# Performance work log

Measured on AMD Instinct MI355X. Metric: run time of the kernel, lower is better.

## Reference

```python
import jax, jax.numpy as jnp
import numpy as np

M, D, A, H, N = 400000, 256, 64, 8, 50000
NEG_SLOPE = 0.2


def setup_inputs() -> dict:
    key = jax.random.key(0)
    ks = jax.random.split(key, 8)
    msg = jax.random.normal(ks[0], (M, D), dtype=jnp.float32)
    index = jax.random.randint(ks[1], (M,), 0, N, dtype=jnp.int32)
    t = jax.random.uniform(ks[2], (M,), dtype=jnp.float32)
    scale = 1.0 / np.sqrt(D).astype(np.float32)
    # per-head Linear(D, A, bias=False) weights, stacked: [H, D, A]
    Wq = jax.random.normal(ks[3], (H, D, A), dtype=jnp.float32) * scale
    Wk = jax.random.normal(ks[4], (H, D, A), dtype=jnp.float32) * scale
    Wv = jax.random.normal(ks[5], (H, D, A), dtype=jnp.float32) * scale
    # out_layer: Linear(H*A, D) with bias
    Wout = jax.random.normal(ks[6], (H * A, D), dtype=jnp.float32) * (1.0 / np.sqrt(H * A).astype(np.float32))
    bout = jax.random.normal(ks[7], (D,), dtype=jnp.float32) * 0.01
    return {"msg": msg, "index": index, "t": t, "dim_size": N,
            "Wq": Wq, "Wk": Wk, "Wv": Wv, "Wout": Wout, "bout": bout}


def _segment_attention(msg, index, dim_size, Wq, Wk, Wv, Wout, bout):
    # per-head projections, all heads at once: [m, H, A]
    q = jnp.einsum('md,hda->mha', msg, Wq)
    k = jnp.einsum('md,hda->mha', msg, Wk)
    v = jnp.einsum('md,hda->mha', msg, Wv)
    # per-head dot-product score: [m, H]
    scores = jnp.sum(q * k, axis=-1)
    scores = jnp.where(scores >= 0, scores, NEG_SLOPE * scores)  # leaky_relu
    # scatter softmax over node segments
    seg_max = jax.ops.segment_max(scores, index, num_segments=dim_size)  # [N, H]
    seg_max = jnp.where(jnp.isfinite(seg_max), seg_max, 0.0)  # empty segments
    e = jnp.exp(scores - seg_max[index])  # [m, H]
    seg_sum = jax.ops.segment_sum(e, index, num_segments=dim_size)  # [N, H]
    attn = e / seg_sum[index]  # [m, H]
    # weighted scatter-sum of values -> [N, H, A]
    out_h = jax.ops.segment_sum(v * attn[..., None], index, num_segments=dim_size)
    # concat heads (head-major order matches torch.cat over head list)
    out = out_h.reshape(dim_size, H * A)
    return out @ Wout + bout  # [N, D]


def reference(msg, index, t, dim_size, Wq, Wk, Wv, Wout, bout):
    # t is accepted but unused, matching the original forward
    return _segment_attention(msg, index, dim_size, Wq, Wk, Wv, Wout, bout)
```

## Files before the change

### kernel.cpp

```cpp
#include <hip/hip_runtime.h>
#include <hip/hip_bf16.h>

typedef _Float16 half8 __attribute__((ext_vector_type(8)));
typedef _Float16 half4 __attribute__((ext_vector_type(4)));
typedef float f32x4 __attribute__((ext_vector_type(4)));


#define MFMA16(a, b, c) __builtin_amdgcn_mfma_f32_16x16x32_f16(a, b, c, 0, 0, 0)

__global__ void k_prep(const float* __restrict__ Wq, const float* __restrict__ Wk,
                       const float* __restrict__ Wv, const float* __restrict__ Wout,
                       _Float16* __restrict__ wqkT, _Float16* __restrict__ CT,
                       const int* __restrict__ index, int* __restrict__ counts, int M)
{
    const int b = blockIdx.x;
    const int t = threadIdx.x;
    if (b < 512) {
        int gid = b * 256 + t;
        int h = gid >> 14;
        int d = (gid >> 6) & 255;
        int a = gid & 63;
        int k0 = d >> 5, lk = (d >> 3) & 3, j = d & 7;
        int cb = a >> 4, lr = a & 15;
        int idx = ((k0 * 4 + cb) * 64 + lk * 16 + lr) * 8 + j;
        wqkT[h * 16384 + idx]       = (_Float16)Wq[gid];
        wqkT[(8 + h) * 16384 + idx] = (_Float16)Wk[gid];
    } else if (b < 1024) {
        __shared__ float wv[4][64];
        int bb = b - 512;
        int h = bb >> 6, din0 = (bb & 63) << 2;
        wv[t >> 6][t & 63] = Wv[((h << 8) + din0 + (t >> 6)) * 64 + (t & 63)];
        __syncthreads();
        float s[4] = {0.f, 0.f, 0.f, 0.f};
        for (int a = 0; a < 64; ++a) {
            float wo = Wout[(h * 64 + a) * 256 + t];
            #pragma unroll
            for (int dd = 0; dd < 4; ++dd) s[dd] += wv[dd][a] * wo;
        }
        int nb = t >> 4, lr = t & 15;
        #pragma unroll
        for (int dd = 0; dd < 4; ++dd) {
            int din = din0 + dd;
            int k0 = din >> 5, lk = (din >> 3) & 3, j = din & 7;
            CT[(size_t)((nb * 8 + h) * 8 + k0) * 512 + (lk * 16 + lr) * 8 + j] = (_Float16)s[dd];
        }
    } else {
        int m = (b - 1024) * 256 + t;
        if (m < M) atomicAdd(&counts[index[m]], 1);
    }
}

__global__ __launch_bounds__(1024) void k_scan1(const int* __restrict__ counts,
                                                int* __restrict__ starts,
                                                int* __restrict__ blocktot, int N) {
    __shared__ int s[1024];
    int b = blockIdx.x, t = threadIdx.x;
    int i = b * 1024 + t;
    int x = (i < N) ? counts[i] : 0;
    s[t] = x;
    __syncthreads();
    #pragma unroll
    for (int off = 1; off < 1024; off <<= 1) {
        int v = (t >= off) ? s[t - off] : 0;
        __syncthreads();
        s[t] += v;
        __syncthreads();
    }
    if (i < N) starts[i] = s[t] - x;
    if (t == 1023) blocktot[b] = s[1023];
}

__global__ void k_scan2(const int* __restrict__ blocktot, int* __restrict__ blockoff, int NC) {
    if (threadIdx.x == 0 && blockIdx.x == 0) {
        int run = 0;
        for (int i = 0; i < NC; ++i) { blockoff[i] = run; run += blocktot[i]; }
    }
}

__global__ __launch_bounds__(1024) void k_scan3(int* __restrict__ starts,
                                                int* __restrict__ cursor,
                                                const int* __restrict__ blockoff,
                                                int N, int M) {
    int b = blockIdx.x, t = threadIdx.x;
    int i = b * 1024 + t;
    if (i < N) {
        int v = starts[i] + blockoff[b];
        starts[i] = v;
        cursor[i] = v;
    }
    if (b == 0 && t == 0) starts[N] = M;
}

__global__ void k_scatteridx(const int* __restrict__ index, int* __restrict__ cursor,
                             int* __restrict__ sorted, int* __restrict__ segsorted, int M) {
    int m = blockIdx.x * 256 + threadIdx.x;
    if (m < M) {
        int idx = index[m];
        int pos = atomicAdd(&cursor[idx], 1);
        sorted[pos] = m;
        segsorted[pos] = idx;
    }
}

__global__ __launch_bounds__(256) void k_zero_bnd(const int* __restrict__ segsorted,
                                                  float* __restrict__ u, int M) {
    long r0 = (long)blockIdx.x * 128;
    int g0 = segsorted[r0];
    int g1 = segsorted[r0 + 127];
    int t = threadIdx.x;
    float4 z = {0.f, 0.f, 0.f, 0.f};
    float4* p0 = (float4*)(u + (long)g0 * 2048);
    float4* p1 = (float4*)(u + (long)g1 * 2048);
    p0[t] = z; p0[t + 256] = z;
    p1[t] = z; p1[t + 256] = z;
}

__device__ __forceinline__ void flush_u(float* __restrict__ u, float* __restrict__ segsum,
                                        int g, int gl0, int ghi, int h, int l,
                                        f32x4 a0, float se)
{
    bool bd = (g == gl0) || (g == ghi);
    float* d0 = u + (long)g * 2048 + h * 256 + l * 4;
    if (bd) {
        atomicAdd(d0 + 0, a0[0]); atomicAdd(d0 + 1, a0[1]);
        atomicAdd(d0 + 2, a0[2]); atomicAdd(d0 + 3, a0[3]);
    } else {
        __builtin_nontemporal_store(a0, (f32x4*)d0);
    }
    if (l == 0) {
        float* ds = segsum + (long)g * 8 + h;
        if (bd) atomicAdd(ds, se); else *ds = se;
    }
}

__global__ __launch_bounds__(512) void k_score_wsum(
    const float* __restrict__ msg, const int* __restrict__ sorted,
    const int* __restrict__ segsorted, const _Float16* __restrict__ wqkT,
    float* __restrict__ u, float* __restrict__ segsum, int M)
{
    __shared__ __align__(16) _Float16 At[128 * 256];
    __shared__ float e_lds[128][9];
    __shared__ int s_id[128];
    __shared__ int s_sg[128];
    char* ldsA = (char*)At;
    const int t = threadIdx.x;

    int nwg = gridDim.x;
    int qc = nwg >> 3, rc = nwg & 7;
    int xcd = blockIdx.x & 7, ofs = blockIdx.x >> 3;
    int blk = ((xcd < rc) ? xcd * (qc + 1) : rc * (qc + 1) + (xcd - rc) * qc) + ofs;
    const long m0 = (long)blk * 128;

    if (t < 128) {
        s_id[t] = sorted[m0 + t];
        s_sg[t] = segsorted[m0 + t];
    }
    __syncthreads();

    const f32x4* msgf4 = (const f32x4*)msg;
    #pragma unroll
    for (int it = 0; it < 16; ++it) {
        int e4 = it * 512 + t;
        int row = e4 >> 6, c4 = e4 & 63;
        f32x4 v = __builtin_nontemporal_load(msgf4 + (long)s_id[row] * 64 + c4);
        half4 hv = {(_Float16)v[0], (_Float16)v[1], (_Float16)v[2], (_Float16)v[3]};
        int bb = ((row << 9) + (c4 << 3)) ^ ((row & 7) << 4);
        *(half4*)(ldsA + bb) = hv;
    }
    __syncthreads();

    const int w = t >> 6, l = t & 63, lr = l & 15, lk = l >> 4;
    const int rh = w & 1;
    const int hp = w >> 1;
    const f32x4 zero = {0.f, 0.f, 0.f, 0.f};

    #pragma unroll 1
    for (int hh = 0; hh < 2; ++hh) {
        const int h = hp + hh * 4;
        const _Float16* wq = wqkT + (size_t)h * 16384;
        const _Float16* wk = wqkT + (size_t)(8 + h) * 16384;

        #pragma unroll 1
        for (int pa = 0; pa < 2; ++pa) {
            const int r0 = rh * 64 + pa * 32 + lr;
            const int r1 = r0 + 16;
            f32x4 pq0 = zero, pq1 = zero;
            __builtin_amdgcn_s_setprio(1);
            #pragma unroll 1
            for (int cb = 0; cb < 4; ++cb) {
                f32x4 aq0 = zero, aq1 = zero, ak0 = zero, ak1 = zero;
                #pragma unroll
                for (int k0 = 0; k0 < 8; ++k0) {
                    int c = k0 * 64 + lk * 16;
                    half8 a0 = *(const half8*)(ldsA + (((r0 << 9) + c) ^ ((r0 & 7) << 4)));
                    half8 a1 = *(const half8*)(ldsA + (((r1 << 9) + c) ^ ((r1 & 7) << 4)));
                    half8 bq = *(const half8*)(wq + ((k0 * 4 + cb) * 64 + l) * 8);
                    half8 bk = *(const half8*)(wk + ((k0 * 4 + cb) * 64 + l) * 8);
                    aq0 = MFMA16(a0, bq, aq0);
                    ak0 = MFMA16(a0, bk, ak0);
                    aq1 = MFMA16(a1, bq, aq1);
                    ak1 = MFMA16(a1, bk, ak1);
                }
                pq0 += aq0 * ak0;
                pq1 += aq1 * ak1;
            }
            __builtin_amdgcn_s_setprio(0);
            #pragma unroll
            for (int off = 1; off < 16; off <<= 1) {
                pq0[0] += __shfl_xor(pq0[0], off); pq0[1] += __shfl_xor(pq0[1], off);
                pq0[2] += __shfl_xor(pq0[2], off); pq0[3] += __shfl_xor(pq0[3], off);
                pq1[0] += __shfl_xor(pq1[0], off); pq1[1] += __shfl_xor(pq1[1], off);
                pq1[2] += __shfl_xor(pq1[2], off); pq1[3] += __shfl_xor(pq1[3], off);
            }
            if (lr == 0) {
                int rb = rh * 64 + pa * 32 + lk * 4;
                #pragma unroll
                for (int j = 0; j < 4; ++j) {
                    float s0 = pq0[j];
                    s0 = (s0 >= 0.f) ? s0 : 0.2f * s0;
                    e_lds[rb + j][h] = __expf(s0);
                    float s1 = pq1[j];
                    s1 = (s1 >= 0.f) ? s1 : 0.2f * s1;
                    e_lds[rb + 16 + j][h] = __expf(s1);
                }
            }
        }
    }
    __syncthreads();

    const int gl0 = s_sg[0], ghi = s_sg[127];
    f32x4 a0 = zero;
    float se = 0.f;
    int cur = gl0;

    #pragma unroll 4
    for (int row = 0; row < 128; ++row) {
        int sg = s_sg[row];
        if (sg != cur) {
            flush_u(u, segsum, cur, gl0, ghi, w, l, a0, se);
            cur = sg; a0 = zero; se = 0.f;
        }
        int bb = ((row << 9) + (l << 3)) ^ ((row & 7) << 4);
        half4 mv = *(const half4*)(ldsA + bb);
        float e = e_lds[row][w];
        a0[0] += e * (float)mv[0];
        a0[1] += e * (float)mv[1];
        a0[2] += e * (float)mv[2];
        a0[3] += e * (float)mv[3];
        se += e;
    }
    flush_u(u, segsum, cur, gl0, ghi, w, l, a0, se);
}

__global__ __launch_bounds__(256, 2) void k_out3(
    const float* __restrict__ u, const float* __restrict__ segsum,
    const _Float16* __restrict__ CT, const float* __restrict__ bout,
    float* __restrict__ out, int N)
{
    const int t = threadIdx.x;
    const int w = t >> 6, l = t & 63, lr = l & 15, lk = l >> 4;
    const long r0 = ((long)blockIdx.x * 4 + w) * 32;
    if (r0 >= N) return;

    const f32x4 zero = {0.f, 0.f, 0.f, 0.f};
    f32x4 ac0[16], ac1[16];
    #pragma unroll
    for (int nb = 0; nb < 16; ++nb) { ac0[nb] = zero; ac1[nb] = zero; }

    long rlo = r0 + lr;      if (rlo > N - 1) rlo = N - 1;
    long rhi = r0 + 16 + lr; if (rhi > N - 1) rhi = N - 1;
    const float* ulo = u + rlo * 2048;
    const float* uhi = u + rhi * 2048;
    const float* sslo = segsum + rlo * 8;
    const float* sshi = segsum + rhi * 8;

    #pragma unroll 1
    for (int kc = 0; kc < 8; ++kc) {
        float s0 = sslo[kc];
        float i0 = (s0 > 0.f) ? 1.f / s0 : 0.f;
        float s1 = sshi[kc];
        float i1 = (s1 > 0.f) ? 1.f / s1 : 0.f;
        #pragma unroll
        for (int k0 = 0; k0 < 8; ++k0) {
            const f32x4* p0 = (const f32x4*)(ulo + kc * 256 + k0 * 32 + lk * 8);
            const f32x4* p1 = (const f32x4*)(uhi + kc * 256 + k0 * 32 + lk * 8);
            f32x4 ua = __builtin_nontemporal_load(p0);
            f32x4 ub = __builtin_nontemporal_load(p0 + 1);
            f32x4 uc = __builtin_nontemporal_load(p1);
            f32x4 ud = __builtin_nontemporal_load(p1 + 1);
            half8 alo = {(_Float16)(ua[0] * i0), (_Float16)(ua[1] * i0),
                         (_Float16)(ua[2] * i0), (_Float16)(ua[3] * i0),
                         (_Float16)(ub[0] * i0), (_Float16)(ub[1] * i0),
                         (_Float16)(ub[2] * i0), (_Float16)(ub[3] * i0)};
            half8 ahi = {(_Float16)(uc[0] * i1), (_Float16)(uc[1] * i1),
                         (_Float16)(uc[2] * i1), (_Float16)(uc[3] * i1),
                         (_Float16)(ud[0] * i1), (_Float16)(ud[1] * i1),
                         (_Float16)(ud[2] * i1), (_Float16)(ud[3] * i1)};
            __builtin_amdgcn_s_setprio(1);
            #pragma unroll
            for (int nb = 0; nb < 16; ++nb) {
                half8 b = *(const half8*)(CT + (size_t)((nb * 8 + kc) * 8 + k0) * 512 + l * 8);
                ac0[nb] = MFMA16(alo, b, ac0[nb]);
                ac1[nb] = MFMA16(ahi, b, ac1[nb]);
            }
            __builtin_amdgcn_s_setprio(0);
        }
    }

    #pragma unroll
    for (int nb = 0; nb < 16; ++nb) {
        int col = nb * 16 + lr;
        float bb = bout[col];
        #pragma unroll
        for (int j = 0; j < 4; ++j) {
            long row = r0 + lk * 4 + j;
            if (row < N) out[row * 256 + col] = ac0[nb][j] + bb;
            long row2 = r0 + 16 + lk * 4 + j;
            if (row2 < N) out[row2 * 256 + col] = ac1[nb][j] + bb;
        }
    }
}

extern "C" void kernel_launch(void* const* d_in, const int* in_sizes, int n_in,
                              void* d_out, int out_size, void* d_ws, size_t ws_size,
                              hipStream_t stream)
{
    const float* msg   = (const float*)d_in[0];
    const int*   index = (const int*)d_in[1];
    const float* Wq    = (const float*)d_in[4];
    const float* Wk    = (const float*)d_in[5];
    const float* Wv    = (const float*)d_in[6];
    const float* Wout  = (const float*)d_in[7];
    const float* bout  = (const float*)d_in[8];
    float* out = (float*)d_out;

    const int M = in_sizes[0] / 256;
    const int N = out_size / 256;
    const int NC = (N + 1023) / 1024;

    char* ws = (char*)d_ws;
    _Float16* wqkT = (_Float16*)(ws);
    _Float16* CT   = (_Float16*)(ws + 524288);
    size_t o2 = 1572864;
    float* segsum = (float*)(ws + o2);
    int* counts   = (int*)(ws + o2 + (size_t)N * 32);
    size_t uoff   = (o2 + (size_t)N * 36 + 255) & ~(size_t)255;
    float* u      = (float*)(ws + uoff);
    size_t p2     = uoff + (size_t)N * 8192;
    int* cursor    = (int*)(ws + p2);
    int* starts    = (int*)(ws + p2 + (size_t)N * 4);
    char* p3       = ws + p2 + (((size_t)N * 8 + 4 + 63) & ~(size_t)63);
    int* sorted    = (int*)(p3);
    int* segsorted = (int*)(p3 + (size_t)M * 4);
    int* blocktot  = (int*)(p3 + (size_t)M * 8);
    int* blockoff  = (int*)(p3 + (size_t)M * 8 + 256);

    hipMemsetAsync(ws + o2, 0, (size_t)N * 36, stream);

    k_prep<<<1024 + (M + 255) / 256, 256, 0, stream>>>(Wq, Wk, Wv, Wout, wqkT, CT,
                                                       index, counts, M);
    k_scan1<<<NC, 1024, 0, stream>>>(counts, starts, blocktot, N);
    k_scan2<<<1, 64, 0, stream>>>(blocktot, blockoff, NC);
    k_scan3<<<NC, 1024, 0, stream>>>(starts, cursor, blockoff, N, M);
    k_scatteridx<<<(M + 255) / 256, 256, 0, stream>>>(index, cursor, sorted, segsorted, M);
    k_zero_bnd<<<M / 128, 256, 0, stream>>>(segsorted, u, M);
    k_score_wsum<<<M / 128, 512, 0, stream>>>(msg, sorted, segsorted, wqkT, u, segsum, M);
    k_out3<<<(N + 127) / 128, 256, 0, stream>>>(u, segsum, CT, bout, out, N);
}
```

Measured before the change: 778.7 us.

## Fold boundary zeroing into scatter and assign one head per wave

Removes the separate boundary-zeroing kernel by having the scatter thread at a tile boundary position zero the segment's accumulator row. It also remaps score computation so each wave handles one head over all rows, which removes the head loop and the block barrier before the weighted sum. The cost is that the zeroing is now done serially by single threads, and the score and weighted-sum phases rely on the same wave producing and consuming its head's exp values.

Result: slower. 878.9 us (+12.9%).

```diff
diff --git a/kernel.cpp b/kernel.cpp
--- a/kernel.cpp
+++ b/kernel.cpp
@@ -92,27 +92,22 @@
 }
 
 __global__ void k_scatteridx(const int* __restrict__ index, int* __restrict__ cursor,
-                             int* __restrict__ sorted, int* __restrict__ segsorted, int M) {
+                             int* __restrict__ sorted, int* __restrict__ segsorted,
+                             float* __restrict__ u, int M) {
     int m = blockIdx.x * 256 + threadIdx.x;
     if (m < M) {
         int idx = index[m];
         int pos = atomicAdd(&cursor[idx], 1);
         sorted[pos] = m;
         segsorted[pos] = idx;
-    }
-}
-
-__global__ __launch_bounds__(256) void k_zero_bnd(const int* __restrict__ segsorted,
-                                                  float* __restrict__ u, int M) {
-    long r0 = (long)blockIdx.x * 128;
-    int g0 = segsorted[r0];
-    int g1 = segsorted[r0 + 127];
-    int t = threadIdx.x;
-    float4 z = {0.f, 0.f, 0.f, 0.f};
-    float4* p0 = (float4*)(u + (long)g0 * 2048);
-    float4* p1 = (float4*)(u + (long)g1 * 2048);
-    p0[t] = z; p0[t + 256] = z;
-    p1[t] = z; p1[t + 256] = z;
+        int pl = pos & 127;
+        if (pl == 0 || pl == 127) {
+            f32x4 z = {0.f, 0.f, 0.f, 0.f};
+            f32x4* p = (f32x4*)(u + (long)idx * 2048);
+            #pragma unroll
+            for (int i = 0; i < 512; ++i) p[i] = z;
+        }
+    }
 }
 
 __device__ __forceinline__ void flush_u(float* __restrict__ u, float* __restrict__ segsum,
@@ -170,63 +165,55 @@
     __syncthreads();
 
     const int w = t >> 6, l = t & 63, lr = l & 15, lk = l >> 4;
-    const int rh = w & 1;
-    const int hp = w >> 1;
     const f32x4 zero = {0.f, 0.f, 0.f, 0.f};
+    const _Float16* wq = wqkT + (size_t)w * 16384;
+    const _Float16* wk = wqkT + (size_t)(8 + w) * 16384;
 
     #pragma unroll 1
-    for (int hh = 0; hh < 2; ++hh) {
-        const int h = hp + hh * 4;
-        const _Float16* wq = wqkT + (size_t)h * 16384;
-        const _Float16* wk = wqkT + (size_t)(8 + h) * 16384;
-
+    for (int pa = 0; pa < 4; ++pa) {
+        const int r0 = pa * 32 + lr;
+        const int r1 = r0 + 16;
+        f32x4 pq0 = zero, pq1 = zero;
+        __builtin_amdgcn_s_setprio(1);
         #pragma unroll 1
-        for (int pa = 0; pa < 2; ++pa) {
-            const int r0 = rh * 64 + pa * 32 + lr;
-            const int r1 = r0 + 16;
-            f32x4 pq0 = zero, pq1 = zero;
-            __builtin_amdgcn_s_setprio(1);
-            #pragma unroll 1
-            for (int cb = 0; cb < 4; ++cb) {
-                f32x4 aq0 = zero, aq1 = zero, ak0 = zero, ak1 = zero;
-                #pragma unroll
-                for (int k0 = 0; k0 < 8; ++k0) {
-                    int c = k0 * 64 + lk * 16;
-                    half8 a0 = *(const half8*)(ldsA + (((r0 << 9) + c) ^ ((r0 & 7) << 4)));
-                    half8 a1 = *(const half8*)(ldsA + (((r1 << 9) + c) ^ ((r1 & 7) << 4)));
-                    half8 bq = *(const half8*)(wq + ((k0 * 4 + cb) * 64 + l) * 8);
-                    half8 bk = *(const half8*)(wk + ((k0 * 4 + cb) * 64 + l) * 8);
-                    aq0 = MFMA16(a0, bq, aq0);
-                    ak0 = MFMA16(a0, bk, ak0);
-                    aq1 = MFMA16(a1, bq, aq1);
-                    ak1 = MFMA16(a1, bk, ak1);
-                }
-                pq0 += aq0 * ak0;
-                pq1 += aq1 * ak1;
+        for (int cb = 0; cb < 4; ++cb) {
+            f32x4 aq0 = zero, aq1 = zero, ak0 = zero, ak1 = zero;
+            #pragma unroll
+            for (int k0 = 0; k0 < 8; ++k0) {
+                int c = k0 * 64 + lk * 16;
+                half8 a0 = *(const half8*)(ldsA + (((r0 << 9) + c) ^ ((r0 & 7) << 4)));
+                half8 a1 = *(const half8*)(ldsA + (((r1 << 9) + c) ^ ((r1 & 7) << 4)));
+                half8 bq = *(const half8*)(wq + ((k0 * 4 + cb) * 64 + l) * 8);
+                half8 bk = *(const half8*)(wk + ((k0 * 4 + cb) * 64 + l) * 8);
+                aq0 = MFMA16(a0, bq, aq0);
+                ak0 = MFMA16(a0, bk, ak0);
+                aq1 = MFMA16(a1, bq, aq1);
+                ak1 = MFMA16(a1, bk, ak1);
             }
-            __builtin_amdgcn_s_setprio(0);
-            #pragma unroll
-            for (int off = 1; off < 16; off <<= 1) {
-                pq0[0] += __shfl_xor(pq0[0], off); pq0[1] += __shfl_xor(pq0[1], off);
-                pq0[2] += __shfl_xor(pq0[2], off); pq0[3] += __shfl_xor(pq0[3], off);
-                pq1[0] += __shfl_xor(pq1[0], off); pq1[1] += __shfl_xor(pq1[1], off);
-                pq1[2] += __shfl_xor(pq1[2], off); pq1[3] += __shfl_xor(pq1[3], off);
+            pq0 += aq0 * ak0;
+            pq1 += aq1 * ak1;
+        }
+        __builtin_amdgcn_s_setprio(0);
+        #pragma unroll
+        for (int off = 1; off < 16; off <<= 1) {
+            pq0[0] += __shfl_xor(pq0[0], off); pq0[1] += __shfl_xor(pq0[1], off);
+            pq0[2] += __shfl_xor(pq0[2], off); pq0[3] += __shfl_xor(pq0[3], off);
+            pq1[0] += __shfl_xor(pq1[0], off); pq1[1] += __shfl_xor(pq1[1], off);
+            pq1[2] += __shfl_xor(pq1[2], off); pq1[3] += __shfl_xor(pq1[3], off);
+        }
+        if (lr == 0) {
+            int rb = pa * 32 + lk * 4;
+            #pragma unroll
+            for (int j = 0; j < 4; ++j) {
+                float s0 = pq0[j];
+                s0 = (s0 >= 0.f) ? s0 : 0.2f * s0;
+                e_lds[rb + j][w] = __expf(s0);
+                float s1 = pq1[j];
+                s1 = (s1 >= 0.f) ? s1 : 0.2f * s1;
+                e_lds[rb + 16 + j][w] = __expf(s1);
             }
-            if (lr == 0) {
-                int rb = rh * 64 + pa * 32 + lk * 4;
-                #pragma unroll
-                for (int j = 0; j < 4; ++j) {
-                    float s0 = pq0[j];
-                    s0 = (s0 >= 0.f) ? s0 : 0.2f * s0;
-                    e_lds[rb + j][h] = __expf(s0);
-                    float s1 = pq1[j];
-                    s1 = (s1 >= 0.f) ? s1 : 0.2f * s1;
-                    e_lds[rb + 16 + j][h] = __expf(s1);
-                }
-            }
-        }
-    }
-    __syncthreads();
+        }
+    }
 
     const int gl0 = s_sg[0], ghi = s_sg[127];
     f32x4 a0 = zero;
@@ -362,8 +349,8 @@
     k_scan1<<<NC, 1024, 0, stream>>>(counts, starts, blocktot, N);
     k_scan2<<<1, 64, 0, stream>>>(blocktot, blockoff, NC);
     k_scan3<<<NC, 1024, 0, stream>>>(starts, cursor, blockoff, N, M);
-    k_scatteridx<<<(M + 255) / 256, 256, 0, stream>>>(index, cursor, sorted, segsorted, M);
-    k_zero_bnd<<<M / 128, 256, 0, stream>>>(segsorted, u, M);
+    k_scatteridx<<<(M + 255) / 256, 256, 0, stream>>>(index, cursor, sorted,
+                                                      segsorted, u, M);
     k_score_wsum<<<M / 128, 512, 0, stream>>>(msg, sorted, segsorted, wqkT, u, segsum, M);
     k_out3<<<(N + 127) / 128, 256, 0, stream>>>(u, segsum, CT, bout, out, N);
 }
```
